# Optimization experiments

Measured on AMD Instinct MI355X. Metric: run time of the kernel, lower is better.

The kernel has to match this reference:

```python
import jax, jax.numpy as jnp
import numpy as np

D_MODEL = 1024
N_HEADS = 16
HEAD_DIM = D_MODEL // N_HEADS
B, L = 2, 2048


def setup_inputs() -> dict:
    key = jax.random.key(0)
    ks = jax.random.split(key, 12)
    s = 1.0 / np.sqrt(D_MODEL)
    inp = {
        'q': jax.random.normal(ks[0], (B, L, D_MODEL), dtype=jnp.float32),
        'k': jax.random.normal(ks[1], (B, L, D_MODEL), dtype=jnp.float32),
        'v': jax.random.normal(ks[2], (B, L, D_MODEL), dtype=jnp.float32),
        'Wq': jax.random.uniform(ks[3], (D_MODEL, D_MODEL), jnp.float32, -s, s),
        'bq': jax.random.uniform(ks[4], (D_MODEL,), jnp.float32, -s, s),
        'Wk': jax.random.uniform(ks[5], (D_MODEL, D_MODEL), jnp.float32, -s, s),
        'bk': jax.random.uniform(ks[6], (D_MODEL,), jnp.float32, -s, s),
        'Wv': jax.random.uniform(ks[7], (D_MODEL, D_MODEL), jnp.float32, -s, s),
        'bv': jax.random.uniform(ks[8], (D_MODEL,), jnp.float32, -s, s),
        'Wo': jax.random.uniform(ks[9], (D_MODEL, D_MODEL), jnp.float32, -s, s),
        'bo': jax.random.uniform(ks[10], (D_MODEL,), jnp.float32, -s, s),
    }
    return inp


def _heads(x):
    # (B, L, D) -> (B, H, L, Dh)
    b, l, _ = x.shape
    return x.reshape(b, l, N_HEADS, HEAD_DIM).transpose(0, 2, 1, 3)


def reference(q, k, v, Wq, bq, Wk, bk, Wv, bv, Wo, bo):
    # Linear projections (torch Linear: x @ W.T + b)
    qh = _heads(q @ Wq.T + bq)
    kh = _heads(k @ Wk.T + bk)
    vh = _heads(v @ Wv.T + bv)
    scale = 1.0 / jnp.sqrt(jnp.asarray(HEAD_DIM, dtype=qh.dtype))
    scores = jnp.einsum('bhqd,bhkd->bhqk', qh, kh) * scale  # (B,H,L,L)
    attn = jax.nn.softmax(scores, axis=-1)
    out = jnp.einsum('bhqk,bhkd->bhqd', attn, vh)
    out = out.transpose(0, 2, 1, 3).reshape(q.shape[0], q.shape[1], D_MODEL)
    return out @ Wo.T + bo
```

## Files before the change

### kernel.cpp

```cpp
#include <hip/hip_runtime.h>

typedef unsigned short u16;
typedef __bf16 bf16x8 __attribute__((ext_vector_type(8)));
typedef float f32x4 __attribute__((ext_vector_type(4)));
typedef float f32x16 __attribute__((ext_vector_type(16)));
typedef unsigned short u16x8 __attribute__((ext_vector_type(8)));
typedef unsigned int u32x2 __attribute__((ext_vector_type(2)));

#define LSEQ 2048
#define DM 1024
#define NH 16
#define HD 64
#define SCALE_Q 0.1803368801111244f

__device__ __forceinline__ u16 f2bf(float f) {
  union { float f; unsigned int u; } x;
  x.f = f;
  unsigned int u = x.u;
  u += 0x7FFFu + ((u >> 16) & 1u);
  return (u16)(u >> 16);
}

__device__ __forceinline__ float fexp2(float x) {
  return __builtin_amdgcn_exp2f(x);
}

__device__ __forceinline__ void async16(const void* g, void* l) {
  __builtin_amdgcn_global_load_lds(
      (const __attribute__((address_space(1))) void*)g,
      (__attribute__((address_space(3))) void*)l, 16, 0, 0);
}

__device__ __forceinline__ f32x4 mfma16(bf16x8 a, bf16x8 b, f32x4 c) {
  return __builtin_amdgcn_mfma_f32_16x16x32_bf16(a, b, c, 0, 0, 0);
}
__device__ __forceinline__ f32x16 mfma32(bf16x8 a, bf16x8 b, f32x16 c) {
  return __builtin_amdgcn_mfma_f32_32x32x16_bf16(a, b, c, 0, 0, 0);
}

__device__ __forceinline__ unsigned cvtpk(float lo, float hi) {
  unsigned r;
  asm("v_cvt_pk_bf16_f32 %0, %1, %2" : "=v"(r) : "v"(lo), "v"(hi));
  return r;
}
__device__ __forceinline__ void pswap(unsigned &a, unsigned &b) {
  asm("v_permlane32_swap_b32 %0, %1" : "+v"(a), "+v"(b));
}
__device__ __forceinline__ bf16x8 mk8(unsigned w0, unsigned w1, unsigned w2, unsigned w3) {
  union { unsigned u[4]; bf16x8 v; } x;
  x.u[0] = w0; x.u[1] = w1; x.u[2] = w2; x.u[3] = w3;
  return x.v;
}
__device__ __forceinline__ f32x16 zero16() {
  f32x16 z;
#pragma unroll
  for (int i = 0; i < 16; ++i) z[i] = 0.f;
  return z;
}

#define WAITBAR4 do { asm volatile("s_waitcnt vmcnt(4) lgkmcnt(0)" ::: "memory"); \
                      __builtin_amdgcn_s_barrier(); } while (0)
#define WAITBAR0 do { asm volatile("s_waitcnt vmcnt(0) lgkmcnt(0)" ::: "memory"); \
                      __builtin_amdgcn_s_barrier(); } while (0)

__global__ __launch_bounds__(256) void cvt7(
    const float* __restrict__ a0, const float* __restrict__ a1,
    const float* __restrict__ a2, const float* __restrict__ a3,
    const float* __restrict__ a4, const float* __restrict__ a5,
    const float* __restrict__ a6,
    u16* __restrict__ b0, u16* __restrict__ b1, u16* __restrict__ b2,
    u16* __restrict__ b3, u16* __restrict__ b4, u16* __restrict__ b5,
    u16* __restrict__ b6)
{
  const int t = blockIdx.y;
  const float* s; u16* d; int n;
  switch (t) {
    case 0: s = a0; d = b0; n = 1 << 22; break;
    case 1: s = a1; d = b1; n = 1 << 22; break;
    case 2: s = a2; d = b2; n = 1 << 22; break;
    case 3: s = a3; d = b3; n = 1 << 20; break;
    case 4: s = a4; d = b4; n = 1 << 20; break;
    case 5: s = a5; d = b5; n = 1 << 20; break;
    default: s = a6; d = b6; n = 1 << 20; break;
  }
  const int i = (blockIdx.x * 256 + threadIdx.x) * 8;
  if (i >= n) return;
  f32x4 f0 = *(const f32x4*)(s + i);
  f32x4 f1 = *(const f32x4*)(s + i + 4);
  u16x8 h;
#pragma unroll
  for (int j = 0; j < 4; ++j) { h[j] = f2bf(f0[j]); h[4 + j] = f2bf(f1[j]); }
  *(u16x8*)(d + i) = h;
}

__global__ __launch_bounds__(256) void gemm_qkv(
    const u16* __restrict__ Xq, const u16* __restrict__ Xk, const u16* __restrict__ Xv,
    const u16* __restrict__ Wqb, const u16* __restrict__ Wkb, const u16* __restrict__ Wvb,
    const float* __restrict__ bq, const float* __restrict__ bk, const float* __restrict__ bv,
    u16* __restrict__ Qp, u16* __restrict__ Kp, u16* __restrict__ Vt)
{
  __shared__ __align__(16) u16 As[3][128 * 32];
  __shared__ __align__(16) u16 Bs[3][128 * 32];

  const int tid = threadIdx.x;
  const int lane = tid & 63;
  const int wid = tid >> 6;
  const int lr = lane & 15, lg = lane >> 4;
  const int wr = wid >> 1, wc = wid & 1;
  const int bm = blockIdx.x;
  const int by = blockIdx.y;
  const int wsel = by >> 3;
  const int bn = by & 7;

  const u16* A    = (wsel == 0) ? Xq  : (wsel == 1) ? Xk  : Xv;
  const u16* Bt   = (wsel == 0) ? Wqb : (wsel == 1) ? Wkb : Wvb;
  const float* bias = (wsel == 0) ? bq : (wsel == 1) ? bk : bv;

  const int r0 = tid >> 2;
  const int c0 = (tid & 3) * 8;
  const size_t arow0 = (size_t)(bm * 128 + r0) * DM;
  const size_t arow1 = (size_t)(bm * 128 + 64 + r0) * DM;
  const size_t brow0 = (size_t)(bn * 128 + r0) * DM;
  const size_t brow1 = (size_t)(bn * 128 + 64 + r0) * DM;

#define GSTAGE(t, buf) do { \
    const int kk_ = (t) * 32; \
    async16(A + arow0 + kk_ + c0, &As[buf][tid * 8]); \
    async16(A + arow1 + kk_ + c0, &As[buf][2048 + tid * 8]); \
    async16(Bt + brow0 + kk_ + c0, &Bs[buf][tid * 8]); \
    async16(Bt + brow1 + kk_ + c0, &Bs[buf][2048 + tid * 8]); \
  } while (0)

  f32x4 acc[4][4];
#pragma unroll
  for (int m = 0; m < 4; ++m)
#pragma unroll
    for (int n = 0; n < 4; ++n) {
      f32x4 z = {0.f, 0.f, 0.f, 0.f};
      acc[m][n] = z;
    }

  GSTAGE(0, 0);
  GSTAGE(1, 1);
  asm volatile("s_waitcnt vmcnt(4)" ::: "memory");
  __builtin_amdgcn_s_barrier();

  int cb = 0;
  for (int kt = 0; kt < 32; ++kt) {
    int sb = cb + 2; if (sb >= 3) sb -= 3;
    if (kt + 2 < 32) GSTAGE(kt + 2, sb);
    bf16x8 af[4], bfr[4];
#pragma unroll
    for (int m = 0; m < 4; ++m)
      af[m] = *(const bf16x8*)&As[cb][(wr * 64 + m * 16 + lr) * 32 + lg * 8];
#pragma unroll
    for (int n = 0; n < 4; ++n)
      bfr[n] = *(const bf16x8*)&Bs[cb][(wc * 64 + n * 16 + lr) * 32 + lg * 8];
    __builtin_amdgcn_s_setprio(1);
#pragma unroll
    for (int m = 0; m < 4; ++m)
#pragma unroll
      for (int n = 0; n < 4; ++n)
        acc[m][n] = mfma16(af[m], bfr[n], acc[m][n]);
    __builtin_amdgcn_s_setprio(0);
    if (kt < 31) {
      if (kt + 2 < 32) { WAITBAR4; } else { WAITBAR0; }
    }
    cb = (cb + 1 == 3) ? 0 : cb + 1;
  }
#undef GSTAGE

  if (wsel < 2) {
    u16* Out = (wsel == 0) ? Qp : Kp;
    const float oscale = (wsel == 0) ? SCALE_Q : 1.0f;
#pragma unroll
    for (int m = 0; m < 4; ++m) {
#pragma unroll
      for (int n = 0; n < 4; ++n) {
        const int col = bn * 128 + wc * 64 + n * 16 + lr;
        const float bv_ = bias[col];
        const int h = col >> 6, d = col & 63;
#pragma unroll
        for (int r = 0; r < 4; ++r) {
          const int row = bm * 128 + wr * 64 + m * 16 + lg * 4 + r;
          const int b = row >> 11, l = row & 2047;
          Out[((size_t)(b * NH + h) * LSEQ + l) * HD + d] =
              f2bf((acc[m][n][r] + bv_) * oscale);
        }
      }
    }
  } else {
    const int row0b = bm * 128 + wr * 64 + lg * 4;
    const int b = (bm * 128) >> 11;
#pragma unroll
    for (int m = 0; m < 4; ++m) {
      const int l0 = (row0b + m * 16) & 2047;
#pragma unroll
      for (int n = 0; n < 4; ++n) {
        const int col = bn * 128 + wc * 64 + n * 16 + lr;
        const float bv_ = bias[col];
        const int h = col >> 6, d = col & 63;
        u32x2 w;
        w[0] = cvtpk(acc[m][n][0] + bv_, acc[m][n][1] + bv_);
        w[1] = cvtpk(acc[m][n][2] + bv_, acc[m][n][3] + bv_);
        *(u32x2*)&Vt[((size_t)(b * NH + h) * HD + d) * LSEQ + l0] = w;
      }
    }
  }
}

__global__ __launch_bounds__(256) void attn_fwd(
    const u16* __restrict__ Qp, const u16* __restrict__ Kp, const u16* __restrict__ Vt,
    u16* __restrict__ ctx)
{
  __shared__ __align__(16) u16 Ks[3][64 * 64];
  __shared__ __align__(16) u16 Vts[3][64 * 64];

  const int tid = threadIdx.x;
  const int wid = tid >> 6;
  const int lane = tid & 63;
  const int lq = lane & 31;
  const int h = lane >> 5;

  const int lid = blockIdx.x + (int)gridDim.x * blockIdx.y;
  const int xcd = lid & 7, slot = lid >> 3;
  const int bh = xcd * 4 + (slot >> 4);
  const int qt = slot & 15;

  const u16* Qb = Qp + (size_t)bh * (LSEQ * HD);
  const u16* Kb = Kp + (size_t)bh * (LSEQ * HD);
  const u16* Vb = Vt + (size_t)bh * (HD * LSEQ);

  const int q0 = qt * 128 + wid * 32;

  bf16x8 qf[4];
#pragma unroll
  for (int dk = 0; dk < 4; ++dk)
    qf[dk] = *(const bf16x8*)(Qb + (size_t)(q0 + lq) * HD + dk * 16 + h * 8);

  float l_run = 0.f;
  f32x16 o0 = zero16(), o1 = zero16();

  const int srow = tid >> 3;
  const int sslot = tid & 7;
  const int sswz = (sslot ^ (srow & 7)) << 3;
  const int ksrc = srow * 64 + sswz;
  const size_t vsrc0 = (size_t)srow * LSEQ + sswz;
  const size_t vsrc1 = (size_t)(srow + 32) * LSEQ + sswz;

#define ASTAGE(t, buf) do { \
    async16(Kb + (t) * 4096 + ksrc, &Ks[buf][tid * 8]); \
    async16(Kb + (t) * 4096 + 2048 + ksrc, &Ks[buf][2048 + tid * 8]); \
    async16(Vb + (t) * 64 + vsrc0, &Vts[buf][tid * 8]); \
    async16(Vb + (t) * 64 + vsrc1, &Vts[buf][2048 + tid * 8]); \
  } while (0)

  ASTAGE(0, 0);
  ASTAGE(1, 1);
  asm volatile("s_waitcnt vmcnt(4)" ::: "memory");
  __builtin_amdgcn_s_barrier();

  int cb = 0;
  for (int kt = 0; kt < LSEQ / 64; ++kt) {
    int sb = cb + 2; if (sb >= 3) sb -= 3;
    if (kt + 2 < LSEQ / 64) ASTAGE(kt + 2, sb);

    f32x16 st0 = zero16(), st1 = zero16();
    __builtin_amdgcn_s_setprio(1);
#pragma unroll
    for (int dk = 0; dk < 4; ++dk) {
      const int g = ((2 * dk + h) ^ (lq & 7)) << 3;
      bf16x8 kf0 = *(const bf16x8*)&Ks[cb][lq * 64 + g];
      bf16x8 kf1 = *(const bf16x8*)&Ks[cb][(32 + lq) * 64 + g];
      st0 = mfma32(kf0, qf[dk], st0);
      st1 = mfma32(kf1, qf[dk], st1);
    }
    __builtin_amdgcn_s_setprio(0);

    float rs = 0.f;
#pragma unroll
    for (int i = 0; i < 16; ++i) { st0[i] = fexp2(st0[i]); rs += st0[i]; }
#pragma unroll
    for (int i = 0; i < 16; ++i) { st1[i] = fexp2(st1[i]); rs += st1[i]; }
    l_run += rs;

    unsigned w[16];
#pragma unroll
    for (int m = 0; m < 4; ++m) {
      w[m * 2 + 0] = cvtpk(st0[4 * m + 0], st0[4 * m + 1]);
      w[m * 2 + 1] = cvtpk(st0[4 * m + 2], st0[4 * m + 3]);
      w[8 + m * 2 + 0] = cvtpk(st1[4 * m + 0], st1[4 * m + 1]);
      w[8 + m * 2 + 1] = cvtpk(st1[4 * m + 2], st1[4 * m + 3]);
    }
#pragma unroll
    for (int n = 0; n < 2; ++n) {
      pswap(w[n * 8 + 0], w[n * 8 + 2]);
      pswap(w[n * 8 + 1], w[n * 8 + 3]);
      pswap(w[n * 8 + 4], w[n * 8 + 6]);
      pswap(w[n * 8 + 5], w[n * 8 + 7]);
    }
    bf16x8 pa[4];
    pa[0] = mk8(w[0], w[1], w[2], w[3]);
    pa[1] = mk8(w[4], w[5], w[6], w[7]);
    pa[2] = mk8(w[8], w[9], w[10], w[11]);
    pa[3] = mk8(w[12], w[13], w[14], w[15]);

    __builtin_amdgcn_s_setprio(1);
#pragma unroll
    for (int ks = 0; ks < 4; ++ks) {
      const int g0g = ((2 * ks + h) ^ (lq & 7)) << 3;
      bf16x8 vf0 = *(const bf16x8*)&Vts[cb][lq * 64 + g0g];
      bf16x8 vf1 = *(const bf16x8*)&Vts[cb][(32 + lq) * 64 + g0g];
      o0 = mfma32(pa[ks], vf0, o0);
      o1 = mfma32(pa[ks], vf1, o1);
    }
    __builtin_amdgcn_s_setprio(0);

    if (kt < LSEQ / 64 - 1) {
      if (kt + 2 < LSEQ / 64) { WAITBAR4; } else { WAITBAR0; }
    }
    cb = (cb + 1 == 3) ? 0 : cb + 1;
  }
#undef ASTAGE

  const int b = bh >> 4, head = bh & 15;
  const float ltot = l_run + __shfl_xor(l_run, 32);
  const float linv = 1.0f / ltot;
#pragma unroll
  for (int reg = 0; reg < 16; ++reg) {
    const int row = (reg & 3) + 8 * (reg >> 2) + 4 * h;
    const float iv = __shfl(linv, row);
    const size_t base = ((size_t)(b * LSEQ + q0 + row)) * DM + head * HD;
    ctx[base + lq] = f2bf(o0[reg] * iv);
    ctx[base + 32 + lq] = f2bf(o1[reg] * iv);
  }
}

__global__ __launch_bounds__(256) void gemm_out(
    const u16* __restrict__ Actx, const u16* __restrict__ Wob,
    const float* __restrict__ bo, float* __restrict__ out)
{
  __shared__ __align__(16) u16 As[3][128 * 32];
  __shared__ __align__(16) u16 Bs[3][128 * 32];

  const int tid = threadIdx.x;
  const int lane = tid & 63;
  const int wid = tid >> 6;
  const int lr = lane & 15, lg = lane >> 4;
  const int wr = wid >> 1, wc = wid & 1;
  const int bm = blockIdx.x;
  const int bn = blockIdx.y;

  const int r0 = tid >> 2;
  const int c0 = (tid & 3) * 8;
  const size_t arow0 = (size_t)(bm * 128 + r0) * DM;
  const size_t arow1 = (size_t)(bm * 128 + 64 + r0) * DM;
  const size_t brow0 = (size_t)(bn * 128 + r0) * DM;
  const size_t brow1 = (size_t)(bn * 128 + 64 + r0) * DM;

#define GSTAGE(t, buf) do { \
    const int kk_ = (t) * 32; \
    async16(Actx + arow0 + kk_ + c0, &As[buf][tid * 8]); \
    async16(Actx + arow1 + kk_ + c0, &As[buf][2048 + tid * 8]); \
    async16(Wob + brow0 + kk_ + c0, &Bs[buf][tid * 8]); \
    async16(Wob + brow1 + kk_ + c0, &Bs[buf][2048 + tid * 8]); \
  } while (0)

  f32x4 acc[4][4];
#pragma unroll
  for (int m = 0; m < 4; ++m)
#pragma unroll
    for (int n = 0; n < 4; ++n) {
      f32x4 z = {0.f, 0.f, 0.f, 0.f};
      acc[m][n] = z;
    }

  GSTAGE(0, 0);
  GSTAGE(1, 1);
  asm volatile("s_waitcnt vmcnt(4)" ::: "memory");
  __builtin_amdgcn_s_barrier();

  int cb = 0;
  for (int kt = 0; kt < 32; ++kt) {
    int sb = cb + 2; if (sb >= 3) sb -= 3;
    if (kt + 2 < 32) GSTAGE(kt + 2, sb);
    bf16x8 af[4], bfr[4];
#pragma unroll
    for (int m = 0; m < 4; ++m)
      af[m] = *(const bf16x8*)&As[cb][(wr * 64 + m * 16 + lr) * 32 + lg * 8];
#pragma unroll
    for (int n = 0; n < 4; ++n)
      bfr[n] = *(const bf16x8*)&Bs[cb][(wc * 64 + n * 16 + lr) * 32 + lg * 8];
    __builtin_amdgcn_s_setprio(1);
#pragma unroll
    for (int m = 0; m < 4; ++m)
#pragma unroll
      for (int n = 0; n < 4; ++n)
        acc[m][n] = mfma16(af[m], bfr[n], acc[m][n]);
    __builtin_amdgcn_s_setprio(0);
    if (kt < 31) {
      if (kt + 2 < 32) { WAITBAR4; } else { WAITBAR0; }
    }
    cb = (cb + 1 == 3) ? 0 : cb + 1;
  }
#undef GSTAGE

#pragma unroll
  for (int m = 0; m < 4; ++m) {
#pragma unroll
    for (int n = 0; n < 4; ++n) {
      const int col = bn * 128 + wc * 64 + n * 16 + lr;
      const float bv_ = bo[col];
#pragma unroll
      for (int r = 0; r < 4; ++r) {
        const int row = bm * 128 + wr * 64 + m * 16 + lg * 4 + r;
        out[(size_t)row * DM + col] = acc[m][n][r] + bv_;
      }
    }
  }
}

extern "C" void kernel_launch(void* const* d_in, const int* in_sizes, int n_in,
                              void* d_out, int out_size, void* d_ws, size_t ws_size,
                              hipStream_t stream) {
  const float* q  = (const float*)d_in[0];
  const float* k  = (const float*)d_in[1];
  const float* v  = (const float*)d_in[2];
  const float* Wq = (const float*)d_in[3];
  const float* bq = (const float*)d_in[4];
  const float* Wk = (const float*)d_in[5];
  const float* bk = (const float*)d_in[6];
  const float* Wv = (const float*)d_in[7];
  const float* bv = (const float*)d_in[8];
  const float* Wo = (const float*)d_in[9];
  const float* bo = (const float*)d_in[10];
  float* out = (float*)d_out;

  u16* ws  = (u16*)d_ws;
  u16* Xqb = ws;
  u16* Xkb = Xqb + (4u << 20);
  u16* Xvb = Xkb + (4u << 20);
  u16* Wqb = Xvb + (4u << 20);
  u16* Wkb = Wqb + (1u << 20);
  u16* Wvb = Wkb + (1u << 20);
  u16* Wob = Wvb + (1u << 20);
  u16* Qp  = Wob + (1u << 20);
  u16* Kp  = Qp + (4u << 20);
  u16* Vt  = Kp + (4u << 20);
  u16* ctx = Xqb;

  cvt7<<<dim3(2048, 7), 256, 0, stream>>>(q, k, v, Wq, Wk, Wv, Wo,
                                          Xqb, Xkb, Xvb, Wqb, Wkb, Wvb, Wob);
  gemm_qkv<<<dim3(32, 24), 256, 0, stream>>>(Xqb, Xkb, Xvb, Wqb, Wkb, Wvb,
                                             bq, bk, bv, Qp, Kp, Vt);
  attn_fwd<<<dim3(16, 32), 256, 0, stream>>>(Qp, Kp, Vt, ctx);
  gemm_out<<<dim3(32, 8), 256, 0, stream>>>(ctx, Wob, bo, out);
}
```

Before: 146.5 us.

## Swizzle GEMM LDS tiles, remap block order, use double-buffered pipeline

Both projection GEMMs now store LDS tiles with an XOR swizzle on the 16-byte chunk index, to cut bank conflicts on the fragment reads. They also launch a flat 1D grid whose index is decoded so consecutive blocks spread across N tiles, aimed at L2/XCD locality. The 3-stage async pipeline with manual vmcnt waits and s_setprio is replaced by a simpler 2-buffer scheme with __syncthreads each iteration. This lowers LDS use per block, but it reduces load/compute overlap and relies on the barrier to cover completion of the async LDS loads.

```diff
diff --git a/kernel.cpp b/kernel.cpp
--- a/kernel.cpp
+++ b/kernel.cpp
@@ -99,16 +99,18 @@
     const float* __restrict__ bq, const float* __restrict__ bk, const float* __restrict__ bv,
     u16* __restrict__ Qp, u16* __restrict__ Kp, u16* __restrict__ Vt)
 {
-  __shared__ __align__(16) u16 As[3][128 * 32];
-  __shared__ __align__(16) u16 Bs[3][128 * 32];
+  __shared__ __align__(16) u16 As[2][128 * 32];
+  __shared__ __align__(16) u16 Bs[2][128 * 32];
 
   const int tid = threadIdx.x;
   const int lane = tid & 63;
   const int wid = tid >> 6;
   const int lr = lane & 15, lg = lane >> 4;
   const int wr = wid >> 1, wc = wid & 1;
-  const int bm = blockIdx.x;
-  const int by = blockIdx.y;
+
+  const int hw = blockIdx.x;
+  const int bm = (hw >> 3) & 31;
+  const int by = 3 * (hw & 7) + (hw >> 8);
   const int wsel = by >> 3;
   const int bn = by & 7;
 
@@ -117,11 +119,13 @@
   const float* bias = (wsel == 0) ? bq : (wsel == 1) ? bk : bv;
 
   const int r0 = tid >> 2;
-  const int c0 = (tid & 3) * 8;
+  const int c0 = ((tid & 3) ^ ((r0 >> 1) & 3)) * 8;
   const size_t arow0 = (size_t)(bm * 128 + r0) * DM;
   const size_t arow1 = (size_t)(bm * 128 + 64 + r0) * DM;
   const size_t brow0 = (size_t)(bn * 128 + r0) * DM;
   const size_t brow1 = (size_t)(bn * 128 + 64 + r0) * DM;
+
+  const int sA = (lg ^ ((lr >> 1) & 3)) << 3;
 
 #define GSTAGE(t, buf) do { \
     const int kk_ = (t) * 32; \
@@ -141,32 +145,24 @@
     }
 
   GSTAGE(0, 0);
-  GSTAGE(1, 1);
-  asm volatile("s_waitcnt vmcnt(4)" ::: "memory");
-  __builtin_amdgcn_s_barrier();
-
-  int cb = 0;
+  __syncthreads();
+
   for (int kt = 0; kt < 32; ++kt) {
-    int sb = cb + 2; if (sb >= 3) sb -= 3;
-    if (kt + 2 < 32) GSTAGE(kt + 2, sb);
+    const int cur = kt & 1, nxt = cur ^ 1;
+    if (kt + 1 < 32) GSTAGE(kt + 1, nxt);
     bf16x8 af[4], bfr[4];
 #pragma unroll
     for (int m = 0; m < 4; ++m)
-      af[m] = *(const bf16x8*)&As[cb][(wr * 64 + m * 16 + lr) * 32 + lg * 8];
+      af[m] = *(const bf16x8*)&As[cur][(wr * 64 + m * 16 + lr) * 32 + sA];
 #pragma unroll
     for (int n = 0; n < 4; ++n)
-      bfr[n] = *(const bf16x8*)&Bs[cb][(wc * 64 + n * 16 + lr) * 32 + lg * 8];
-    __builtin_amdgcn_s_setprio(1);
+      bfr[n] = *(const bf16x8*)&Bs[cur][(wc * 64 + n * 16 + lr) * 32 + sA];
 #pragma unroll
     for (int m = 0; m < 4; ++m)
 #pragma unroll
       for (int n = 0; n < 4; ++n)
         acc[m][n] = mfma16(af[m], bfr[n], acc[m][n]);
-    __builtin_amdgcn_s_setprio(0);
-    if (kt < 31) {
-      if (kt + 2 < 32) { WAITBAR4; } else { WAITBAR0; }
-    }
-    cb = (cb + 1 == 3) ? 0 : cb + 1;
+    __syncthreads();
   }
 #undef GSTAGE
 
@@ -340,23 +336,27 @@
     const u16* __restrict__ Actx, const u16* __restrict__ Wob,
     const float* __restrict__ bo, float* __restrict__ out)
 {
-  __shared__ __align__(16) u16 As[3][128 * 32];
-  __shared__ __align__(16) u16 Bs[3][128 * 32];
+  __shared__ __align__(16) u16 As[2][128 * 32];
+  __shared__ __align__(16) u16 Bs[2][128 * 32];
 
   const int tid = threadIdx.x;
   const int lane = tid & 63;
   const int wid = tid >> 6;
   const int lr = lane & 15, lg = lane >> 4;
   const int wr = wid >> 1, wc = wid & 1;
-  const int bm = blockIdx.x;
-  const int bn = blockIdx.y;
+
+  const int hw = blockIdx.x;
+  const int bn = hw & 7;
+  const int bm = hw >> 3;
 
   const int r0 = tid >> 2;
-  const int c0 = (tid & 3) * 8;
+  const int c0 = ((tid & 3) ^ ((r0 >> 1) & 3)) * 8;
   const size_t arow0 = (size_t)(bm * 128 + r0) * DM;
   const size_t arow1 = (size_t)(bm * 128 + 64 + r0) * DM;
   const size_t brow0 = (size_t)(bn * 128 + r0) * DM;
   const size_t brow1 = (size_t)(bn * 128 + 64 + r0) * DM;
+
+  const int sA = (lg ^ ((lr >> 1) & 3)) << 3;
 
 #define GSTAGE(t, buf) do { \
     const int kk_ = (t) * 32; \
@@ -376,32 +376,24 @@
     }
 
   GSTAGE(0, 0);
-  GSTAGE(1, 1);
-  asm volatile("s_waitcnt vmcnt(4)" ::: "memory");
-  __builtin_amdgcn_s_barrier();
-
-  int cb = 0;
+  __syncthreads();
+
   for (int kt = 0; kt < 32; ++kt) {
-    int sb = cb + 2; if (sb >= 3) sb -= 3;
-    if (kt + 2 < 32) GSTAGE(kt + 2, sb);
+    const int cur = kt & 1, nxt = cur ^ 1;
+    if (kt + 1 < 32) GSTAGE(kt + 1, nxt);
     bf16x8 af[4], bfr[4];
 #pragma unroll
     for (int m = 0; m < 4; ++m)
-      af[m] = *(const bf16x8*)&As[cb][(wr * 64 + m * 16 + lr) * 32 + lg * 8];
+      af[m] = *(const bf16x8*)&As[cur][(wr * 64 + m * 16 + lr) * 32 + sA];
 #pragma unroll
     for (int n = 0; n < 4; ++n)
-      bfr[n] = *(const bf16x8*)&Bs[cb][(wc * 64 + n * 16 + lr) * 32 + lg * 8];
-    __builtin_amdgcn_s_setprio(1);
+      bfr[n] = *(const bf16x8*)&Bs[cur][(wc * 64 + n * 16 + lr) * 32 + sA];
 #pragma unroll
     for (int m = 0; m < 4; ++m)
 #pragma unroll
       for (int n = 0; n < 4; ++n)
         acc[m][n] = mfma16(af[m], bfr[n], acc[m][n]);
-    __builtin_amdgcn_s_setprio(0);
-    if (kt < 31) {
-      if (kt + 2 < 32) { WAITBAR4; } else { WAITBAR0; }
-    }
-    cb = (cb + 1 == 3) ? 0 : cb + 1;
+    __syncthreads();
   }
 #undef GSTAGE
 
@@ -451,8 +443,8 @@
 
   cvt7<<<dim3(2048, 7), 256, 0, stream>>>(q, k, v, Wq, Wk, Wv, Wo,
                                           Xqb, Xkb, Xvb, Wqb, Wkb, Wvb, Wob);
-  gemm_qkv<<<dim3(32, 24), 256, 0, stream>>>(Xqb, Xkb, Xvb, Wqb, Wkb, Wvb,
-                                             bq, bk, bv, Qp, Kp, Vt);
+  gemm_qkv<<<768, 256, 0, stream>>>(Xqb, Xkb, Xvb, Wqb, Wkb, Wvb,
+                                    bq, bk, bv, Qp, Kp, Vt);
   attn_fwd<<<dim3(16, 32), 256, 0, stream>>>(Qp, Kp, Vt, ctx);
-  gemm_out<<<dim3(32, 8), 256, 0, stream>>>(ctx, Wob, bo, out);
-}
+  gemm_out<<<256, 256, 0, stream>>>(ctx, Wob, bo, out);
+}
```

Result: no change. 147.9 us (+1.0%).
